# Optimization experiments

Hardware: AMD Instinct MI355X
Metric: run time of the kernel (lower is better)

## Reference

```python
import jax, jax.numpy as jnp
import numpy as np

B, H = 8, 8
C_IN, C_OUT = 128, 128
E, O = C_IN // H, C_OUT // H              # per-head channels
S = (32, 32, 64)                           # spatial dims (space_dims_q == space_dims_kv)
M = (8, 8, 8)                              # lowest-mode block kept per rfft dim
N_MODES = M[0] * M[1] * M[2]               # 512 = mask.sum()
SCALE = 1.0 / (C_IN * C_OUT)


def setup_inputs() -> dict:
    key = jax.random.key(0)
    k1, k2, k3, k4 = jax.random.split(key, 4)
    q = jax.random.normal(k1, (B, H, E) + S, dtype=jnp.float32)
    k = jax.random.normal(k2, (B, H, E) + S, dtype=jnp.float32)
    # torch.rand(..., dtype=cfloat): real and imag parts each uniform [0,1), scaled
    w_re = jax.random.uniform(k3, (H, E, O, N_MODES), dtype=jnp.float32) * SCALE
    w_im = jax.random.uniform(k4, (H, E, O, N_MODES), dtype=jnp.float32) * SCALE
    return {"q": q, "k": k, "w_re": w_re, "w_im": w_im}


def _select_modes(x_ft):
    # block low-mode mask -> slice + flatten (C order, matches torch bool indexing)
    m0, m1, m2 = M
    return x_ft[..., :m0, :m1, :m2].reshape(x_ft.shape[:3] + (-1,))


def reference(q, k, w_re, w_im):
    m0, m1, m2 = M
    xq_ft = jnp.fft.rfftn(q, axes=(3, 4, 5), norm='ortho')   # [B,H,E,32,32,33] c64
    xk_ft = jnp.fft.rfftn(k, axes=(3, 4, 5), norm='ortho')
    xq_sel = _select_modes(xq_ft)                             # [B,H,E,Mq]
    xk_sel = _select_modes(xk_ft)                             # [B,H,E,Mkv]
    w = jax.lax.complex(w_re, w_im)                           # [H,E,O,Mq]

    # complex attention: no conjugation, complex tanh (matches torch)
    att = jnp.tanh(jnp.einsum('bhex,bhey->bhxy', xq_sel, xk_sel))
    xqkv = jnp.einsum('bhxy,bhey->bhex', att, xk_sel)         # [B,H,E,Mq]
    xqkvw = jnp.einsum('bhex,heox->bhox', xqkv, w)            # [B,H,O,Mq]

    out_ft = jnp.zeros((q.shape[0], H, O, S[0], S[1], S[2] // 2 + 1),
                       dtype=xqkvw.dtype)
    out_ft = out_ft.at[..., :m0, :m1, :m2].set(
        xqkvw.reshape(q.shape[0], H, O, m0, m1, m2))

    # canonical_fft_freq over dims (3,4): x <- (x + conj(x[-i mod s0, -j mod s1]))/2
    neg = jnp.roll(jnp.flip(out_ft, axis=(3, 4)), shift=(1, 1), axis=(3, 4))
    out_ft = (out_ft + jnp.conj(neg)) * 0.5

    out = jnp.fft.irfftn(out_ft / (C_IN * C_OUT), axes=(3, 4, 5), s=S, norm='ortho')
    return out  # original returns (out, None)
```

## Files before the change

kernel.cpp:

```cpp
#include <hip/hip_runtime.h>

#define PI_F 3.14159265358979323846f

template<int v> struct ic_t { static constexpr int value = v; };

template<int N, int I = 0, typename F>
__device__ __forceinline__ void sfor(F&& f) {
  if constexpr (I < N) { f(ic_t<I>{}); sfor<N, I + 1>(static_cast<F&&>(f)); }
}

__host__ __device__ constexpr int fold_idx(int t) {
  t &= 63;
  return (t <= 16) ? t : (t <= 32) ? (32 - t) : (t <= 48) ? (t - 32) : (64 - t);
}
__host__ __device__ constexpr float fold_sgn(int t) {
  t &= 63;
  return (t <= 16) ? 1.f : (t <= 48) ? -1.f : 1.f;
}

#define TCOS(T) (fold_sgn(T) * cc[fold_idx(T)])
#define TSIN(T) (fold_sgn(((T) + 48) & 63) * cc[fold_idx(((T) + 48) & 63)])

__global__ __launch_bounds__(256, 2)
void k1_fwd_dft(const float* __restrict__ qg, const float* __restrict__ kg,
                float2* __restrict__ qsel, float2* __restrict__ ksel)
{
  __shared__ float AhR[8 * 577];
  __shared__ float AhI[8 * 577];
  __shared__ float BrL[32 * 68];
  __shared__ float BiL[32 * 68];
  __shared__ float2 tw32s[32];

  const int tid = threadIdx.x;
  const int bid = blockIdx.x;
  const int t1023 = bid & 1023;
  const float* __restrict__ src = (bid < 1024 ? qg : kg) + (size_t)t1023 * 65536;
  float2* __restrict__ dst = (bid < 1024 ? qsel : ksel) + t1023 * 512;

  float cc[17];
  sfor<17>([&](auto J) { constexpr int j = decltype(J)::value;
    cc[j] = cosf((float)j * (PI_F / 32.f)); });

  if (tid < 32) {
    float s, c;
    sincosf((float)tid * (2.f * PI_F / 32.f), &s, &c);
    tw32s[tid] = make_float2(c, s);
  }

  for (int hf = 0; hf < 2; ++hf) {
    for (int rr = 0; rr < 2; ++rr) {
      const int row = hf * 512 + rr * 256 + tid;
      const int n0h = (row >> 5) & 15;
      const int n1 = row & 31;
      const float4* __restrict__ rp = (const float4*)(src + (size_t)row * 64);
      float g0[16], g2[16], g1r[16], g1i[16];
      sfor<4>([&](auto JC) {
        constexpr int j = decltype(JC)::value;
        const float4 va = rp[j];
        const float4 vb = rp[4 + j];
        const float4 vc = rp[8 + j];
        const float4 vd = rp[12 + j];
        sfor<4>([&](auto MC) {
          constexpr int m = decltype(MC)::value;
          constexpr int r = 4 * j + m;
          const float xa = (m == 0) ? va.x : (m == 1) ? va.y : (m == 2) ? va.z : va.w;
          const float xb = (m == 0) ? vb.x : (m == 1) ? vb.y : (m == 2) ? vb.z : vb.w;
          const float xc = (m == 0) ? vc.x : (m == 1) ? vc.y : (m == 2) ? vc.z : vc.w;
          const float xd = (m == 0) ? vd.x : (m == 1) ? vd.y : (m == 2) ? vd.z : vd.w;
          const float s02 = xa + xc, d02 = xa - xc;
          const float s13 = xb + xd, d31 = xd - xb;
          g0[r] = s02 + s13; g2[r] = s02 - s13;
          g1r[r] = d02;      g1i[r] = d31;
        });
      });
      float Xr[8], Xi[8];
      sfor<8>([&](auto K) { Xr[decltype(K)::value] = 0.f; Xi[decltype(K)::value] = 0.f; });
      sfor<16>([&](auto RC) {
        constexpr int r = decltype(RC)::value;
        Xr[0] += g0[r];
        sfor<3>([&](auto EC) {
          constexpr int k2 = 2 * (decltype(EC)::value + 1);
          constexpr int t = (k2 * r) & 63;
          const float g = (k2 == 4) ? g0[r] : g2[r];
          Xr[k2] = fmaf(g,  TCOS(t), Xr[k2]);
          Xi[k2] = fmaf(-g, TSIN(t), Xi[k2]);
        });
        sfor<4>([&](auto UC) {
          constexpr int k2 = 2 * decltype(UC)::value + 1;
          constexpr int t = (k2 * r) & 63;
          const float gr = g1r[r];
          const float gi = ((k2 & 3) == 1) ? g1i[r] : -g1i[r];
          Xr[k2] = fmaf(gr, TCOS(t), fmaf(gi,  TSIN(t), Xr[k2]));
          Xi[k2] = fmaf(gi, TCOS(t), fmaf(-gr, TSIN(t), Xi[k2]));
        });
      });
      const int abase = n0h * 36 + n1;
      sfor<8>([&](auto K) {
        constexpr int k2 = decltype(K)::value;
        AhR[k2 * 577 + abase] = Xr[k2];
        AhI[k2 * 577 + abase] = Xi[k2];
      });
    }
    __syncthreads();
    if (tid < 128) {
      const int n0h = tid >> 3;
      const int k2 = tid & 7;
      const int n0 = hf * 16 + n0h;
      float br[8], bi[8];
      sfor<8>([&](auto K) { br[decltype(K)::value] = 0.f; bi[decltype(K)::value] = 0.f; });
      const int base = k2 * 577 + n0h * 36;
      sfor<32>([&](auto NC) {
        constexpr int n1 = decltype(NC)::value;
        const float ar = AhR[base + n1];
        const float ai = AhI[base + n1];
        sfor<8>([&](auto KC) {
          constexpr int k1 = decltype(KC)::value;
          constexpr int t = (2 * k1 * n1) & 63;
          br[k1] = fmaf(ar, TCOS(t), fmaf(ai,  TSIN(t), br[k1]));
          bi[k1] = fmaf(ai, TCOS(t), fmaf(-ar, TSIN(t), bi[k1]));
        });
      });
      sfor<8>([&](auto KC) {
        constexpr int k1 = decltype(KC)::value;
        BrL[n0 * 68 + k1 * 8 + k2] = br[k1];
        BiL[n0 * 68 + k1 * 8 + k2] = bi[k1];
      });
    }
    __syncthreads();
  }

  {
    const int lane = tid & 63;
    const int wv = tid >> 6;
    const int k1 = lane >> 3;
    const int k2 = lane & 7;
    #pragma unroll
    for (int j = 0; j < 2; ++j) {
      const int k0 = wv * 2 + j;
      float xr = 0.f, xi = 0.f;
      #pragma unroll 8
      for (int n0 = 0; n0 < 32; ++n0) {
        const float br = BrL[n0 * 68 + k1 * 8 + k2];
        const float bi = BiL[n0 * 68 + k1 * 8 + k2];
        const float2 w = tw32s[(k0 * n0) & 31];
        xr = fmaf(br, w.x, fmaf(bi,  w.y, xr));
        xi = fmaf(bi, w.x, fmaf(-br, w.y, xi));
      }
      dst[(k0 << 6) + (k1 << 3) + k2] =
          make_float2(xr * (1.f / 256.f), xi * (1.f / 256.f));
    }
  }
}

__global__ __launch_bounds__(256, 2)
void k2_attn(const float2* __restrict__ qsel, const float2* __restrict__ ksel,
             float2* __restrict__ xqkv)
{
  __shared__ float2 Kl[8192];
  const int tid = threadIdx.x;
  const int bh = blockIdx.x >> 2;
  const int xq = blockIdx.x & 3;

  const float2* __restrict__ kb = ksel + bh * 8192;
  for (int i = tid; i < 8192; i += 256) Kl[i] = kb[i];

  const int xr = tid & 127;
  const int yh = tid >> 7;
  const int x = xq * 128 + xr;
  const float2* __restrict__ qb = qsel + bh * 8192;
  float qr[16], qi[16], ar[16], ai[16];
  sfor<16>([&](auto E) {
    constexpr int e = decltype(E)::value;
    const float2 v = qb[e * 512 + x];
    qr[e] = v.x; qi[e] = v.y;
    ar[e] = 0.f; ai[e] = 0.f;
  });
  __syncthreads();

  const int y0 = yh * 256;
  for (int y = y0; y < y0 + 256; ++y) {
    float kr[16], ki[16];
    float sr = 0.f, si = 0.f;
    sfor<16>([&](auto E) {
      constexpr int e = decltype(E)::value;
      const float2 v = Kl[e * 512 + y];
      kr[e] = v.x; ki[e] = v.y;
      sr = fmaf(qr[e], v.x, fmaf(-qi[e], v.y, sr));
      si = fmaf(qr[e], v.y, fmaf( qi[e], v.x, si));
    });
    float a2 = 2.f * sr;
    a2 = fminf(fmaxf(a2, -30.f), 30.f);
    const float b2 = 2.f * si;
    const float ea = expf(a2);
    const float ei = 1.f / ea;
    const float sh = 0.5f * (ea - ei);
    const float chp = 0.5f * (ea + ei);
    float sb, cb;
    sincosf(b2, &sb, &cb);
    const float inv = 1.f / (chp + cb);
    const float tr = sh * inv;
    const float ti = sb * inv;
    sfor<16>([&](auto E) {
      constexpr int e = decltype(E)::value;
      ar[e] = fmaf(tr, kr[e], fmaf(-ti, ki[e], ar[e]));
      ai[e] = fmaf(tr, ki[e], fmaf( ti, kr[e], ai[e]));
    });
  }
  __syncthreads();
  float* __restrict__ red = (float*)Kl;
  if (yh) {
    sfor<16>([&](auto E) {
      constexpr int e = decltype(E)::value;
      red[e * 128 + xr] = ar[e];
      red[2048 + e * 128 + xr] = ai[e];
    });
  }
  __syncthreads();
  if (!yh) {
    float2* __restrict__ ob = xqkv + bh * 8192;
    sfor<16>([&](auto E) {
      constexpr int e = decltype(E)::value;
      ob[e * 512 + x] = make_float2(ar[e] + red[e * 128 + xr],
                                    ai[e] + red[2048 + e * 128 + xr]);
    });
  }
}

#define SCALE_OUT (1.f / 4194304.f)

__global__ __launch_bounds__(256, 2)
void k3_inv(const float2* __restrict__ xqkv, const float* __restrict__ w_re,
            const float* __restrict__ w_im, float* __restrict__ out)
{
  __shared__ float2 Fs[512];
  __shared__ float cn[64];
  __shared__ float Ur[4096], Ui[4096];
  __shared__ float Vr[2048], Vi[2048];

  const int tid = threadIdx.x;
  const int bho = blockIdx.x;
  const int o = bho & 15;
  const int h = (bho >> 4) & 7;
  const int bh = bho >> 4;

  if (tid < 64) cn[tid] = cosf((float)tid * (PI_F / 32.f));

  float cc[17];
  sfor<17>([&](auto J) { constexpr int j = decltype(J)::value;
    cc[j] = cosf((float)j * (PI_F / 32.f)); });

  const float2* __restrict__ xb = xqkv + bh * 8192;
  const float* __restrict__ wrb = w_re + ((size_t)(h * 256 + o)) * 512;
  const float* __restrict__ wib = w_im + ((size_t)(h * 256 + o)) * 512;
  for (int x = tid; x < 512; x += 256) {
    float fr = 0.f, fi = 0.f;
    sfor<16>([&](auto E) {
      constexpr int e = decltype(E)::value;
      const float2 v = xb[e * 512 + x];
      const float wr = wrb[e * 8192 + x];
      const float wi = wib[e * 8192 + x];
      fr = fmaf(v.x, wr, fmaf(-v.y, wi, fr));
      fi = fmaf(v.x, wi, fmaf( v.y, wr, fi));
    });
    Fs[x] = make_float2(fr * SCALE_OUT, fi * SCALE_OUT);
  }
  __syncthreads();

  const int n2 = tid & 63;
  const int wv = tid >> 6;

  #pragma unroll
  for (int i = 0; i < 16; ++i) {
    const int p = wv * 16 + i;
    float ur = 0.f, ui = 0.f;
    sfor<8>([&](auto KC) {
      constexpr int k2 = decltype(KC)::value;
      const float2 f = Fs[p * 8 + k2];
      const float cv = cn[(k2 * n2) & 63];
      const float wgt = (k2 == 0) ? cv : 2.f * cv;
      ur = fmaf(wgt, f.x, ur);
      ui = fmaf(wgt, f.y, ui);
    });
    Ur[p * 64 + n2] = ur;
    Ui[p * 64 + n2] = ui;
  }
  __syncthreads();

  float u_r[2][8], u_i[2][8];
  sfor<2>([&](auto JC) {
    constexpr int j = decltype(JC)::value;
    sfor<8>([&](auto KC) {
      constexpr int k1 = decltype(KC)::value;
      const int p = (wv * 2 + j) * 8 + k1;
      u_r[j][k1] = Ur[p * 64 + n2];
      u_i[j][k1] = Ui[p * 64 + n2];
    });
  });

  float* __restrict__ ob = out + (size_t)bho * 65536;

  for (int chq = 0; chq < 8; ++chq) {
    sfor<2>([&](auto JC) {
      constexpr int j = decltype(JC)::value;
      const int k0 = wv * 2 + j;
      sfor<4>([&](auto LC) {
        constexpr int l = decltype(LC)::value;
        const int n1 = chq * 4 + l;
        float vr = 0.f, vi = 0.f;
        sfor<8>([&](auto KC) {
          constexpr int k1 = decltype(KC)::value;
          const int t = (2 * k1 * n1) & 63;
          const float cv = cn[t];
          const float sv = cn[(t + 48) & 63];
          vr = fmaf(u_r[j][k1], cv, fmaf(-u_i[j][k1], sv, vr));
          vi = fmaf(u_r[j][k1], sv, fmaf( u_i[j][k1], cv, vi));
        });
        Vr[(k0 * 4 + l) * 64 + n2] = vr;
        Vi[(k0 * 4 + l) * 64 + n2] = vi;
      });
    });
    __syncthreads();
    {
      const int l = wv;
      float vrr[8], vii[8];
      sfor<8>([&](auto KC) {
        constexpr int k0 = decltype(KC)::value;
        vrr[k0] = Vr[(k0 * 4 + l) * 64 + n2];
        vii[k0] = Vi[(k0 * 4 + l) * 64 + n2];
      });
      const int n1 = chq * 4 + l;
      float* __restrict__ op = ob + n1 * 64 + n2;
      sfor<32>([&](auto NC) {
        constexpr int n0 = decltype(NC)::value;
        float acc = vrr[0];
        sfor<7>([&](auto KC) {
          constexpr int k0 = decltype(KC)::value + 1;
          constexpr int t = (2 * k0 * n0) & 63;
          acc = fmaf(vrr[k0], TCOS(t), fmaf(-vii[k0], TSIN(t), acc));
        });
        op[n0 * 2048] = acc;
      });
    }
    __syncthreads();
  }
}

extern "C" void kernel_launch(void* const* d_in, const int* in_sizes, int n_in,
                              void* d_out, int out_size, void* d_ws, size_t ws_size,
                              hipStream_t stream)
{
  (void)in_sizes; (void)n_in; (void)out_size; (void)ws_size;
  const float* q    = (const float*)d_in[0];
  const float* k    = (const float*)d_in[1];
  const float* w_re = (const float*)d_in[2];
  const float* w_im = (const float*)d_in[3];
  float* out = (float*)d_out;

  float2* qsel = (float2*)d_ws;
  float2* ksel = qsel + 1024 * 512;
  float2* xqkv = ksel + 1024 * 512;

  hipLaunchKernelGGL(k1_fwd_dft, dim3(2048), dim3(256), 0, stream, q, k, qsel, ksel);
  hipLaunchKernelGGL(k2_attn,    dim3(256),  dim3(256), 0, stream, qsel, ksel, xqkv);
  hipLaunchKernelGGL(k3_inv,     dim3(1024), dim3(256), 0, stream, xqkv, w_re, w_im, out);
}
```

Measured before the change: 362.6 us.

## Restructure forward DFT loop order and widen attention y-split across more threads

The forward DFT kernel is reordered to transform along the outer dimension first. Each lane reads a column with coalesced strided loads and accumulates k0 modes, then applies the n1 twiddle via shared memory in chunks, and finishes the innermost axis with a 64-thread pass. Shared memory use drops and launch bounds rise to 4 blocks per CU. The attention kernel now uses 512 blocks of 512 threads, splitting y eight ways with a larger shared-memory reduction to raise parallelism, at the cost of extra reduction traffic and a serial final stage in one wave of k1.

```diff
diff --git a/kernel.cpp b/kernel.cpp
--- a/kernel.cpp
+++ b/kernel.cpp
@@ -21,17 +21,16 @@
 #define TCOS(T) (fold_sgn(T) * cc[fold_idx(T)])
 #define TSIN(T) (fold_sgn(((T) + 48) & 63) * cc[fold_idx(((T) + 48) & 63)])
 
-__global__ __launch_bounds__(256, 2)
+__global__ __launch_bounds__(256, 4)
 void k1_fwd_dft(const float* __restrict__ qg, const float* __restrict__ kg,
                 float2* __restrict__ qsel, float2* __restrict__ ksel)
 {
-  __shared__ float AhR[8 * 577];
-  __shared__ float AhI[8 * 577];
-  __shared__ float BrL[32 * 68];
-  __shared__ float BiL[32 * 68];
-  __shared__ float2 tw32s[32];
+  __shared__ float2 Abuf[64 * 65];
+  __shared__ float2 tw32[32];
 
   const int tid = threadIdx.x;
+  const int lane = tid & 63;
+  const int wv = tid >> 6;
   const int bid = blockIdx.x;
   const int t1023 = bid & 1023;
   const float* __restrict__ src = (bid < 1024 ? qg : kg) + (size_t)t1023 * 65536;
@@ -44,129 +43,115 @@
   if (tid < 32) {
     float s, c;
     sincosf((float)tid * (2.f * PI_F / 32.f), &s, &c);
-    tw32s[tid] = make_float2(c, s);
-  }
-
-  for (int hf = 0; hf < 2; ++hf) {
-    for (int rr = 0; rr < 2; ++rr) {
-      const int row = hf * 512 + rr * 256 + tid;
-      const int n0h = (row >> 5) & 15;
-      const int n1 = row & 31;
-      const float4* __restrict__ rp = (const float4*)(src + (size_t)row * 64);
-      float g0[16], g2[16], g1r[16], g1i[16];
-      sfor<4>([&](auto JC) {
-        constexpr int j = decltype(JC)::value;
-        const float4 va = rp[j];
-        const float4 vb = rp[4 + j];
-        const float4 vc = rp[8 + j];
-        const float4 vd = rp[12 + j];
-        sfor<4>([&](auto MC) {
-          constexpr int m = decltype(MC)::value;
-          constexpr int r = 4 * j + m;
-          const float xa = (m == 0) ? va.x : (m == 1) ? va.y : (m == 2) ? va.z : va.w;
-          const float xb = (m == 0) ? vb.x : (m == 1) ? vb.y : (m == 2) ? vb.z : vb.w;
-          const float xc = (m == 0) ? vc.x : (m == 1) ? vc.y : (m == 2) ? vc.z : vc.w;
-          const float xd = (m == 0) ? vd.x : (m == 1) ? vd.y : (m == 2) ? vd.z : vd.w;
-          const float s02 = xa + xc, d02 = xa - xc;
-          const float s13 = xb + xd, d31 = xd - xb;
-          g0[r] = s02 + s13; g2[r] = s02 - s13;
-          g1r[r] = d02;      g1i[r] = d31;
+    tw32[tid] = make_float2(c, s);
+  }
+
+  float Br[2][8], Bi[2][8];
+  sfor<2>([&](auto J) { constexpr int j = decltype(J)::value;
+    sfor<8>([&](auto K) { constexpr int k = decltype(K)::value;
+      Br[j][k] = 0.f; Bi[j][k] = 0.f; }); });
+
+  sfor<4>([&](auto CH) {
+    constexpr int chunk = decltype(CH)::value;
+    sfor<2>([&](auto JC) {
+      constexpr int j = decltype(JC)::value;
+      const int n1 = chunk * 8 + wv * 2 + j;
+      const float* __restrict__ rp = src + n1 * 64 + lane;
+      float accR[8], accI[8];
+      sfor<8>([&](auto K) { constexpr int k = decltype(K)::value;
+        accR[k] = 0.f; accI[k] = 0.f; });
+      sfor<16>([&](auto NP) {
+        constexpr int n0p = decltype(NP)::value;
+        const float a = rp[n0p * 2048];
+        const float b = rp[(n0p + 16) * 2048];
+        const float s = a + b;
+        const float d = a - b;
+        sfor<8>([&](auto KC) {
+          constexpr int k0 = decltype(KC)::value;
+          constexpr int t = (2 * k0 * n0p) & 63;
+          const float g = ((k0 & 1) == 0) ? s : d;
+          accR[k0] = fmaf(g,  TCOS(t), accR[k0]);
+          accI[k0] = fmaf(-g, TSIN(t), accI[k0]);
         });
       });
-      float Xr[8], Xi[8];
-      sfor<8>([&](auto K) { Xr[decltype(K)::value] = 0.f; Xi[decltype(K)::value] = 0.f; });
-      sfor<16>([&](auto RC) {
-        constexpr int r = decltype(RC)::value;
-        Xr[0] += g0[r];
-        sfor<3>([&](auto EC) {
-          constexpr int k2 = 2 * (decltype(EC)::value + 1);
-          constexpr int t = (k2 * r) & 63;
-          const float g = (k2 == 4) ? g0[r] : g2[r];
-          Xr[k2] = fmaf(g,  TCOS(t), Xr[k2]);
-          Xi[k2] = fmaf(-g, TSIN(t), Xi[k2]);
+      const int abase = (wv * 2 + j) * 8 * 64 + lane;
+      sfor<8>([&](auto KC) {
+        constexpr int k0 = decltype(KC)::value;
+        Abuf[abase + k0 * 64] = make_float2(accR[k0], accI[k0]);
+      });
+    });
+    __syncthreads();
+    sfor<2>([&](auto JC) {
+      constexpr int j = decltype(JC)::value;
+      const int k1 = wv * 2 + j;
+      sfor<8>([&](auto NL) {
+        constexpr int n1loc = decltype(NL)::value;
+        constexpr int n1 = chunk * 8 + n1loc;
+        const float2 tw = tw32[(k1 * n1) & 31];
+        sfor<8>([&](auto KC) {
+          constexpr int k0 = decltype(KC)::value;
+          const float2 a = Abuf[(n1loc * 8 + k0) * 64 + lane];
+          Br[j][k0] = fmaf(a.x, tw.x, fmaf( a.y, tw.y, Br[j][k0]));
+          Bi[j][k0] = fmaf(a.y, tw.x, fmaf(-a.x, tw.y, Bi[j][k0]));
         });
-        sfor<4>([&](auto UC) {
-          constexpr int k2 = 2 * decltype(UC)::value + 1;
-          constexpr int t = (k2 * r) & 63;
-          const float gr = g1r[r];
-          const float gi = ((k2 & 3) == 1) ? g1i[r] : -g1i[r];
-          Xr[k2] = fmaf(gr, TCOS(t), fmaf(gi,  TSIN(t), Xr[k2]));
-          Xi[k2] = fmaf(gi, TCOS(t), fmaf(-gr, TSIN(t), Xi[k2]));
-        });
-      });
-      const int abase = n0h * 36 + n1;
-      sfor<8>([&](auto K) {
-        constexpr int k2 = decltype(K)::value;
-        AhR[k2 * 577 + abase] = Xr[k2];
-        AhI[k2 * 577 + abase] = Xi[k2];
-      });
-    }
+      });
+    });
     __syncthreads();
-    if (tid < 128) {
-      const int n0h = tid >> 3;
-      const int k2 = tid & 7;
-      const int n0 = hf * 16 + n0h;
-      float br[8], bi[8];
-      sfor<8>([&](auto K) { br[decltype(K)::value] = 0.f; bi[decltype(K)::value] = 0.f; });
-      const int base = k2 * 577 + n0h * 36;
-      sfor<32>([&](auto NC) {
-        constexpr int n1 = decltype(NC)::value;
-        const float ar = AhR[base + n1];
-        const float ai = AhI[base + n1];
-        sfor<8>([&](auto KC) {
-          constexpr int k1 = decltype(KC)::value;
-          constexpr int t = (2 * k1 * n1) & 63;
-          br[k1] = fmaf(ar, TCOS(t), fmaf(ai,  TSIN(t), br[k1]));
-          bi[k1] = fmaf(ai, TCOS(t), fmaf(-ar, TSIN(t), bi[k1]));
-        });
-      });
+  });
+
+  sfor<2>([&](auto JC) {
+    constexpr int j = decltype(JC)::value;
+    sfor<8>([&](auto KC) {
+      constexpr int k0 = decltype(KC)::value;
+      Abuf[((wv * 2 + j) * 8 + k0) * 65 + lane] = make_float2(Br[j][k0], Bi[j][k0]);
+    });
+  });
+  __syncthreads();
+
+  if (tid < 64) {
+    const float2* __restrict__ rb = &Abuf[tid * 65];
+    float oR[8], oI[8];
+    sfor<8>([&](auto K) { constexpr int k = decltype(K)::value;
+      oR[k] = 0.f; oI[k] = 0.f; });
+    sfor<32>([&](auto MC) {
+      constexpr int m = decltype(MC)::value;
+      const float2 p = rb[m];
+      const float2 q = rb[m + 32];
+      const float sx = p.x + q.x, sy = p.y + q.y;
+      const float dx = p.x - q.x, dy = p.y - q.y;
       sfor<8>([&](auto KC) {
-        constexpr int k1 = decltype(KC)::value;
-        BrL[n0 * 68 + k1 * 8 + k2] = br[k1];
-        BiL[n0 * 68 + k1 * 8 + k2] = bi[k1];
-      });
-    }
-    __syncthreads();
-  }
-
-  {
-    const int lane = tid & 63;
-    const int wv = tid >> 6;
-    const int k1 = lane >> 3;
-    const int k2 = lane & 7;
-    #pragma unroll
-    for (int j = 0; j < 2; ++j) {
-      const int k0 = wv * 2 + j;
-      float xr = 0.f, xi = 0.f;
-      #pragma unroll 8
-      for (int n0 = 0; n0 < 32; ++n0) {
-        const float br = BrL[n0 * 68 + k1 * 8 + k2];
-        const float bi = BiL[n0 * 68 + k1 * 8 + k2];
-        const float2 w = tw32s[(k0 * n0) & 31];
-        xr = fmaf(br, w.x, fmaf(bi,  w.y, xr));
-        xi = fmaf(bi, w.x, fmaf(-br, w.y, xi));
-      }
+        constexpr int k2 = decltype(KC)::value;
+        constexpr int t = (k2 * m) & 63;
+        const float gx = ((k2 & 1) == 0) ? sx : dx;
+        const float gy = ((k2 & 1) == 0) ? sy : dy;
+        oR[k2] = fmaf(gx, TCOS(t), fmaf( gy, TSIN(t), oR[k2]));
+        oI[k2] = fmaf(gy, TCOS(t), fmaf(-gx, TSIN(t), oI[k2]));
+      });
+    });
+    const int k1 = tid >> 3, k0 = tid & 7;
+    sfor<8>([&](auto KC) {
+      constexpr int k2 = decltype(KC)::value;
       dst[(k0 << 6) + (k1 << 3) + k2] =
-          make_float2(xr * (1.f / 256.f), xi * (1.f / 256.f));
-    }
-  }
-}
-
-__global__ __launch_bounds__(256, 2)
+          make_float2(oR[k2] * (1.f / 256.f), oI[k2] * (1.f / 256.f));
+    });
+  }
+}
+
+__global__ __launch_bounds__(512, 4)
 void k2_attn(const float2* __restrict__ qsel, const float2* __restrict__ ksel,
              float2* __restrict__ xqkv)
 {
   __shared__ float2 Kl[8192];
   const int tid = threadIdx.x;
-  const int bh = blockIdx.x >> 2;
-  const int xq = blockIdx.x & 3;
+  const int bh = blockIdx.x >> 3;
+  const int xo = blockIdx.x & 7;
 
   const float2* __restrict__ kb = ksel + bh * 8192;
-  for (int i = tid; i < 8192; i += 256) Kl[i] = kb[i];
-
-  const int xr = tid & 127;
-  const int yh = tid >> 7;
-  const int x = xq * 128 + xr;
+  for (int i = tid; i < 8192; i += 512) Kl[i] = kb[i];
+
+  const int xr = tid & 63;
+  const int yh = tid >> 6;
+  const int x = xo * 64 + xr;
   const float2* __restrict__ qb = qsel + bh * 8192;
   float qr[16], qi[16], ar[16], ai[16];
   sfor<16>([&](auto E) {
@@ -177,8 +162,8 @@
   });
   __syncthreads();
 
-  const int y0 = yh * 256;
-  for (int y = y0; y < y0 + 256; ++y) {
+  const int y0 = yh * 64;
+  for (int y = y0; y < y0 + 64; ++y) {
     float kr[16], ki[16];
     float sr = 0.f, si = 0.f;
     sfor<16>([&](auto E) {
@@ -209,10 +194,11 @@
   __syncthreads();
   float* __restrict__ red = (float*)Kl;
   if (yh) {
-    sfor<16>([&](auto E) {
-      constexpr int e = decltype(E)::value;
-      red[e * 128 + xr] = ar[e];
-      red[2048 + e * 128 + xr] = ai[e];
+    const int g = yh - 1;
+    sfor<16>([&](auto E) {
+      constexpr int e = decltype(E)::value;
+      red[(g * 32 + 2 * e) * 64 + xr] = ar[e];
+      red[(g * 32 + 2 * e + 1) * 64 + xr] = ai[e];
     });
   }
   __syncthreads();
@@ -220,8 +206,13 @@
     float2* __restrict__ ob = xqkv + bh * 8192;
     sfor<16>([&](auto E) {
       constexpr int e = decltype(E)::value;
-      ob[e * 512 + x] = make_float2(ar[e] + red[e * 128 + xr],
-                                    ai[e] + red[2048 + e * 128 + xr]);
+      float sr2 = ar[e], si2 = ai[e];
+      #pragma unroll
+      for (int g = 0; g < 7; ++g) {
+        sr2 += red[(g * 32 + 2 * e) * 64 + xr];
+        si2 += red[(g * 32 + 2 * e + 1) * 64 + xr];
+      }
+      ob[e * 512 + x] = make_float2(sr2, si2);
     });
   }
 }
@@ -361,6 +352,6 @@
   float2* xqkv = ksel + 1024 * 512;
 
   hipLaunchKernelGGL(k1_fwd_dft, dim3(2048), dim3(256), 0, stream, q, k, qsel, ksel);
-  hipLaunchKernelGGL(k2_attn,    dim3(256),  dim3(256), 0, stream, qsel, ksel, xqkv);
+  hipLaunchKernelGGL(k2_attn,    dim3(512),  dim3(512), 0, stream, qsel, ksel, xqkv);
   hipLaunchKernelGGL(k3_inv,     dim3(1024), dim3(256), 0, stream, xqkv, w_re, w_im, out);
 }
```

New measurement: 535.9 us. 1.48x slower.
